# Kernel optimization log

Hardware: AMD Instinct MI355X
Metric: run time of the kernel (lower is better)

The kernel has to match this reference:

```python
import jax, jax.numpy as jnp
import numpy as np

M = 4096   # nodes per layer (also number of input nodes)
L = 32     # internal layers
K = 64     # in-degree of each internal node


def setup_inputs() -> dict:
    key = jax.random.key(0)
    k_x, k_wi, k_bi, k_w, k_b, k_g = jax.random.split(key, 6)
    x = jax.random.normal(k_x, (M, 1), dtype=jnp.float32)
    w_in = jax.random.normal(k_wi, (M, 1), dtype=jnp.float32)
    b_in = jax.random.normal(k_bi, (M,), dtype=jnp.float32)
    # scale internal weights so sigmoid(K-term dot) is not fully saturated
    w = jax.random.normal(k_w, (L, M, K), dtype=jnp.float32) * 0.05
    b = jax.random.normal(k_b, (L, M), dtype=jnp.float32)
    # predecessor indices into the previous layer's value vector
    igraf = jax.random.randint(k_g, (L, M, K), 0, M, dtype=jnp.int32)
    return {"x": x, "w_in": w_in, "b_in": b_in, "w": w, "b": b, "igraf": igraf}


def reference(x, w_in, b_in, w, b, igraf):
    # input nodes: relu(Linear(1,1)) applied to each scalar input, vectorized
    v = jax.nn.relu(w_in[:, 0] * x[:, 0] + b_in)          # [M]
    # internal nodes, layer by layer (topological order):
    # each node gathers K predecessor values and applies sigmoid(Linear(K,1))
    for l in range(L):
        g = v[igraf[l]]                                   # [M, K] irregular gather
        v = jax.nn.sigmoid(jnp.einsum('mk,mk->m', w[l], g) + b[l])
    # original returns values[n_nodes - 1] (shape [1])
    return v[-1:]
```

## Files before the change

### kernel.cpp

```cpp
#include <hip/hip_runtime.h>

#define M 4096
#define L 32
#define K 64
#define NBLK 256
#define BLOCK 256
#define NPW 4
#define NPB 16
#define MK (M * K)
#define FB 0xAAAAAAAAu

__global__ __launch_bounds__(BLOCK)
void net_kernel(const float* __restrict__ x,
                const float* __restrict__ w_in,
                const float* __restrict__ b_in,
                const float* __restrict__ w,
                const float* __restrict__ b,
                const int* __restrict__ igraf,
                float* __restrict__ out,
                unsigned long long* __restrict__ buf)
{
    __shared__ float sv[2][M];

    const int tid  = threadIdx.x;
    const int blk  = blockIdx.x;
    const int wave = tid >> 6;
    const int lane = tid & 63;
    const int base = blk * NPB + wave * NPW;
    const bool lastblk = (blk == NBLK - 1);

    float wv[NPW]; int iv[NPW]; float breg = 0.0f;
    {
        const size_t b0 = (size_t)base * K + (size_t)lane;
        #pragma unroll
        for (int j = 0; j < NPW; ++j) {
            wv[j] = w[b0 + (size_t)j * K];
            iv[j] = igraf[b0 + (size_t)j * K];
        }
        if (lane < NPW) breg = b[base + lane];
    }

    #pragma unroll
    for (int j = 0; j < 4; ++j) {
        const int idx = tid + j * BLOCK;
        const float4 x4 = ((const float4*)x)[idx];
        const float4 wi = ((const float4*)w_in)[idx];
        const float4 bi = ((const float4*)b_in)[idx];
        float4 r;
        r.x = fmaxf(fmaf(wi.x, x4.x, bi.x), 0.0f);
        r.y = fmaxf(fmaf(wi.y, x4.y, bi.y), 0.0f);
        r.z = fmaxf(fmaf(wi.z, x4.z, bi.z), 0.0f);
        r.w = fmaxf(fmaf(wi.w, x4.w, bi.w), 0.0f);
        ((float4*)sv[0])[idx] = r;
    }
    __syncthreads();

    int cur = 0;
    for (int l = 0; l < L; ++l) {
        float p[NPW];
        #pragma unroll
        for (int j = 0; j < NPW; ++j) p[j] = wv[j] * sv[cur][iv[j]];

        #pragma unroll
        for (int j = 0; j < NPW; ++j) {
            #pragma unroll
            for (int off = 32; off > 0; off >>= 1)
                p[j] += __shfl_xor(p[j], off, 64);
        }

        float pj = p[0];
        pj = (lane == 1) ? p[1] : pj;
        pj = (lane == 2) ? p[2] : pj;
        pj = (lane == 3) ? p[3] : pj;
        const float val = 1.0f / (1.0f + __expf(-(pj + breg)));

        if (l == L - 1) {
            if (wave == 3 && lane == 3) out[0] = val;
            break;
        }

        const unsigned tag = FB + (unsigned)(l + 1);
        unsigned long long* bufr = buf + (size_t)((l + 1) & 1) * M;

        if (lane < NPW) {
            const unsigned long long pk =
                ((unsigned long long)tag << 32) |
                (unsigned long long)__float_as_uint(val);
            __hip_atomic_store(&bufr[base + lane], pk,
                               __ATOMIC_RELAXED, __HIP_MEMORY_SCOPE_AGENT);
        }

        if ((l == L - 2) && !lastblk) return;

        unsigned long long vals[16];
        #pragma unroll
        for (int j = 0; j < 16; ++j)
            vals[j] = __hip_atomic_load(&bufr[tid + j * BLOCK],
                                        __ATOMIC_RELAXED,
                                        __HIP_MEMORY_SCOPE_AGENT);

        if ((l + 2 < L) || lastblk) {
            const size_t nb = (size_t)(l + 1) * MK + (size_t)base * K + (size_t)lane;
            #pragma unroll
            for (int j = 0; j < NPW; ++j) {
                wv[j] = w[nb + (size_t)j * K];
                iv[j] = igraf[nb + (size_t)j * K];
            }
            if (lane < NPW) breg = b[(l + 1) * M + base + lane];
        }

        for (;;) {
            bool ok = true;
            #pragma unroll
            for (int j = 0; j < 16; ++j) {
                if ((unsigned)(vals[j] >> 32) != tag) {
                    ok = false;
                    vals[j] = __hip_atomic_load(&bufr[tid + j * BLOCK],
                                                __ATOMIC_RELAXED,
                                                __HIP_MEMORY_SCOPE_AGENT);
                }
            }
            if (ok) break;
            __builtin_amdgcn_s_sleep(1);
        }

        const int nxt = cur ^ 1;
        #pragma unroll
        for (int j = 0; j < 16; ++j)
            sv[nxt][tid + j * BLOCK] = __uint_as_float((unsigned)vals[j]);

        __syncthreads();
        cur = nxt;
    }
}

extern "C" void kernel_launch(void* const* d_in, const int* in_sizes, int n_in,
                              void* d_out, int out_size, void* d_ws, size_t ws_size,
                              hipStream_t stream) {
    const float* x     = (const float*)d_in[0];
    const float* w_in  = (const float*)d_in[1];
    const float* b_in  = (const float*)d_in[2];
    const float* wt    = (const float*)d_in[3];
    const float* b     = (const float*)d_in[4];
    const int*   igraf = (const int*)d_in[5];
    float*       out   = (float*)d_out;

    unsigned long long* buf = (unsigned long long*)d_ws;

    hipLaunchKernelGGL(net_kernel, dim3(NBLK), dim3(BLOCK), 0, stream,
                       x, w_in, b_in, wt, b, igraf, out, buf);
    (void)in_sizes; (void)n_in; (void)out_size; (void)ws_size;
}
```

Before: 189.8 us.

## Use fewer, larger blocks and prefetch weights several layers ahead

```diff
diff --git a/kernel.cpp b/kernel.cpp
--- a/kernel.cpp
+++ b/kernel.cpp
@@ -3,10 +3,11 @@
 #define M 4096
 #define L 32
 #define K 64
-#define NBLK 256
-#define BLOCK 256
+#define NBLK 64
+#define BLOCK 1024
 #define NPW 4
-#define NPB 16
+#define NPB 64
+#define D 4
 #define MK (M * K)
 #define FB 0xAAAAAAAAu
 
@@ -27,110 +28,126 @@
     const int wave = tid >> 6;
     const int lane = tid & 63;
     const int base = blk * NPB + wave * NPW;
-    const bool lastblk = (blk == NBLK - 1);
+    const bool finblk = (blk == NBLK - 1);
 
-    float wv[NPW]; int iv[NPW]; float breg = 0.0f;
-    {
-        const size_t b0 = (size_t)base * K + (size_t)lane;
+    float4 x4[4], wi[4], bi[4];
+    #pragma unroll
+    for (int j = 0; j < 4; ++j) {
+        const int idx = tid + j * BLOCK;
+        x4[j] = ((const float4*)x)[idx];
+        wi[j] = ((const float4*)w_in)[idx];
+        bi[j] = ((const float4*)b_in)[idx];
+    }
+    __asm__ volatile("" ::: "memory");
+
+    float wbuf[D][NPW]; int ibuf[D][NPW]; float bbuf[D];
+    #pragma unroll
+    for (int d = 0; d < D; ++d) {
+        const size_t o = (size_t)d * MK + (size_t)base * K + (size_t)lane;
         #pragma unroll
         for (int j = 0; j < NPW; ++j) {
-            wv[j] = w[b0 + (size_t)j * K];
-            iv[j] = igraf[b0 + (size_t)j * K];
+            wbuf[d][j] = w[o + (size_t)j * K];
+            ibuf[d][j] = igraf[o + (size_t)j * K];
         }
-        if (lane < NPW) breg = b[base + lane];
+        bbuf[d] = (lane < NPW) ? b[d * M + base + lane] : 0.0f;
     }
 
     #pragma unroll
     for (int j = 0; j < 4; ++j) {
         const int idx = tid + j * BLOCK;
-        const float4 x4 = ((const float4*)x)[idx];
-        const float4 wi = ((const float4*)w_in)[idx];
-        const float4 bi = ((const float4*)b_in)[idx];
         float4 r;
-        r.x = fmaxf(fmaf(wi.x, x4.x, bi.x), 0.0f);
-        r.y = fmaxf(fmaf(wi.y, x4.y, bi.y), 0.0f);
-        r.z = fmaxf(fmaf(wi.z, x4.z, bi.z), 0.0f);
-        r.w = fmaxf(fmaf(wi.w, x4.w, bi.w), 0.0f);
+        r.x = fmaxf(fmaf(wi[j].x, x4[j].x, bi[j].x), 0.0f);
+        r.y = fmaxf(fmaf(wi[j].y, x4[j].y, bi[j].y), 0.0f);
+        r.z = fmaxf(fmaf(wi[j].z, x4[j].z, bi[j].z), 0.0f);
+        r.w = fmaxf(fmaf(wi[j].w, x4[j].w, bi[j].w), 0.0f);
         ((float4*)sv[0])[idx] = r;
     }
     __syncthreads();
 
     int cur = 0;
-    for (int l = 0; l < L; ++l) {
-        float p[NPW];
+    for (int g = 0; g < L / D; ++g) {
         #pragma unroll
-        for (int j = 0; j < NPW; ++j) p[j] = wv[j] * sv[cur][iv[j]];
+        for (int s = 0; s < D; ++s) {
+            const int l = g * D + s;
 
-        #pragma unroll
-        for (int j = 0; j < NPW; ++j) {
+            float p[NPW];
             #pragma unroll
-            for (int off = 32; off > 0; off >>= 1)
-                p[j] += __shfl_xor(p[j], off, 64);
-        }
+            for (int j = 0; j < NPW; ++j)
+                p[j] = wbuf[s][j] * sv[cur][ibuf[s][j]];
 
-        float pj = p[0];
-        pj = (lane == 1) ? p[1] : pj;
-        pj = (lane == 2) ? p[2] : pj;
-        pj = (lane == 3) ? p[3] : pj;
-        const float val = 1.0f / (1.0f + __expf(-(pj + breg)));
-
-        if (l == L - 1) {
-            if (wave == 3 && lane == 3) out[0] = val;
-            break;
-        }
-
-        const unsigned tag = FB + (unsigned)(l + 1);
-        unsigned long long* bufr = buf + (size_t)((l + 1) & 1) * M;
-
-        if (lane < NPW) {
-            const unsigned long long pk =
-                ((unsigned long long)tag << 32) |
-                (unsigned long long)__float_as_uint(val);
-            __hip_atomic_store(&bufr[base + lane], pk,
-                               __ATOMIC_RELAXED, __HIP_MEMORY_SCOPE_AGENT);
-        }
-
-        if ((l == L - 2) && !lastblk) return;
-
-        unsigned long long vals[16];
-        #pragma unroll
-        for (int j = 0; j < 16; ++j)
-            vals[j] = __hip_atomic_load(&bufr[tid + j * BLOCK],
-                                        __ATOMIC_RELAXED,
-                                        __HIP_MEMORY_SCOPE_AGENT);
-
-        if ((l + 2 < L) || lastblk) {
-            const size_t nb = (size_t)(l + 1) * MK + (size_t)base * K + (size_t)lane;
             #pragma unroll
             for (int j = 0; j < NPW; ++j) {
-                wv[j] = w[nb + (size_t)j * K];
-                iv[j] = igraf[nb + (size_t)j * K];
+                #pragma unroll
+                for (int off = 32; off > 0; off >>= 1)
+                    p[j] += __shfl_xor(p[j], off, 64);
             }
-            if (lane < NPW) breg = b[(l + 1) * M + base + lane];
+
+            float pj = p[0];
+            pj = (lane == 1) ? p[1] : pj;
+            pj = (lane == 2) ? p[2] : pj;
+            pj = (lane == 3) ? p[3] : pj;
+            const float val = 1.0f / (1.0f + __expf(-(pj + bbuf[s])));
+
+            if (l == L - 1) {
+                if (wave == 15 && lane == 3) out[0] = val;
+                return;
+            }
+
+            const unsigned tag = FB + (unsigned)(l + 1);
+            unsigned long long* bufr = buf + (size_t)((l + 1) & 1) * M;
+
+            if (lane < NPW) {
+                const unsigned long long pk =
+                    ((unsigned long long)tag << 32) |
+                    (unsigned long long)__float_as_uint(val);
+                __hip_atomic_store(&bufr[base + lane], pk,
+                                   __ATOMIC_RELAXED, __HIP_MEMORY_SCOPE_AGENT);
+            }
+
+            if (l == L - 2 && !finblk) return;
+
+            unsigned long long vals[4];
+            #pragma unroll
+            for (int j = 0; j < 4; ++j)
+                vals[j] = __hip_atomic_load(&bufr[tid + j * BLOCK],
+                                            __ATOMIC_RELAXED,
+                                            __HIP_MEMORY_SCOPE_AGENT);
+            __asm__ volatile("" ::: "memory");
+
+            if (l + D < L) {
+                const size_t o = (size_t)(l + D) * MK
+                               + (size_t)base * K + (size_t)lane;
+                #pragma unroll
+                for (int j = 0; j < NPW; ++j) {
+                    wbuf[s][j] = w[o + (size_t)j * K];
+                    ibuf[s][j] = igraf[o + (size_t)j * K];
+                }
+                if (lane < NPW) bbuf[s] = b[(l + D) * M + base + lane];
+            }
+
+            for (;;) {
+                bool ok = true;
+                #pragma unroll
+                for (int j = 0; j < 4; ++j) {
+                    if ((unsigned)(vals[j] >> 32) != tag) {
+                        ok = false;
+                        vals[j] = __hip_atomic_load(&bufr[tid + j * BLOCK],
+                                                    __ATOMIC_RELAXED,
+                                                    __HIP_MEMORY_SCOPE_AGENT);
+                    }
+                }
+                if (ok) break;
+                __builtin_amdgcn_s_sleep(1);
+            }
+
+            const int nxt = cur ^ 1;
+            #pragma unroll
+            for (int j = 0; j < 4; ++j)
+                sv[nxt][tid + j * BLOCK] =
+                    __uint_as_float((unsigned)vals[j]);
+            __syncthreads();
+            cur = nxt;
         }
-
-        for (;;) {
-            bool ok = true;
-            #pragma unroll
-            for (int j = 0; j < 16; ++j) {
-                if ((unsigned)(vals[j] >> 32) != tag) {
-                    ok = false;
-                    vals[j] = __hip_atomic_load(&bufr[tid + j * BLOCK],
-                                                __ATOMIC_RELAXED,
-                                                __HIP_MEMORY_SCOPE_AGENT);
-                }
-            }
-            if (ok) break;
-            __builtin_amdgcn_s_sleep(1);
-        }
-
-        const int nxt = cur ^ 1;
-        #pragma unroll
-        for (int j = 0; j < 16; ++j)
-            sv[nxt][tid + j * BLOCK] = __uint_as_float((unsigned)vals[j]);
-
-        __syncthreads();
-        cur = nxt;
     }
 }
 
```

Measured after the change: 221.4 us. 16.7% more time.

## Replace per-value tagged polling with per-block flags and layer-indexed buffers

Applied to the files above, without the earlier changes.

```diff
diff --git a/kernel.cpp b/kernel.cpp
--- a/kernel.cpp
+++ b/kernel.cpp
@@ -8,7 +8,6 @@
 #define NPW 4
 #define NPB 16
 #define MK (M * K)
-#define FB 0xAAAAAAAAu
 
 __global__ __launch_bounds__(BLOCK)
 void net_kernel(const float* __restrict__ x,
@@ -18,7 +17,8 @@
                 const float* __restrict__ b,
                 const int* __restrict__ igraf,
                 float* __restrict__ out,
-                unsigned long long* __restrict__ buf)
+                unsigned char* __restrict__ flags,
+                float* __restrict__ bufs)
 {
     __shared__ float sv[2][M];
 
@@ -76,28 +76,25 @@
 
         if (l == L - 1) {
             if (wave == 3 && lane == 3) out[0] = val;
-            break;
+            return;
         }
 
-        const unsigned tag = FB + (unsigned)(l + 1);
-        unsigned long long* bufr = buf + (size_t)((l + 1) & 1) * M;
+        const int r = l + 1;
+        float* bufr = bufs + (size_t)r * M;
 
         if (lane < NPW) {
-            const unsigned long long pk =
-                ((unsigned long long)tag << 32) |
-                (unsigned long long)__float_as_uint(val);
-            __hip_atomic_store(&bufr[base + lane], pk,
+            float old = __hip_atomic_exchange(&bufr[base + lane], val,
+                                              __ATOMIC_RELAXED,
+                                              __HIP_MEMORY_SCOPE_AGENT);
+            __asm__ volatile("" :: "v"(old));
+        }
+        __syncthreads();
+
+        if (tid == 0)
+            __hip_atomic_store(&flags[blk], (unsigned char)r,
                                __ATOMIC_RELAXED, __HIP_MEMORY_SCOPE_AGENT);
-        }
 
-        if ((l == L - 2) && !lastblk) return;
-
-        unsigned long long vals[16];
-        #pragma unroll
-        for (int j = 0; j < 16; ++j)
-            vals[j] = __hip_atomic_load(&bufr[tid + j * BLOCK],
-                                        __ATOMIC_RELAXED,
-                                        __HIP_MEMORY_SCOPE_AGENT);
+        if (l == L - 2 && !lastblk) return;
 
         if ((l + 2 < L) || lastblk) {
             const size_t nb = (size_t)(l + 1) * MK + (size_t)base * K + (size_t)lane;
@@ -109,26 +106,24 @@
             if (lane < NPW) breg = b[(l + 1) * M + base + lane];
         }
 
-        for (;;) {
-            bool ok = true;
-            #pragma unroll
-            for (int j = 0; j < 16; ++j) {
-                if ((unsigned)(vals[j] >> 32) != tag) {
-                    ok = false;
-                    vals[j] = __hip_atomic_load(&bufr[tid + j * BLOCK],
-                                                __ATOMIC_RELAXED,
-                                                __HIP_MEMORY_SCOPE_AGENT);
-                }
+        {
+            const unsigned tgt = 0x01010101u * (unsigned)r;
+            const unsigned* f4 = (const unsigned*)flags;
+            for (;;) {
+                const unsigned v = __hip_atomic_load(&f4[lane],
+                        __ATOMIC_RELAXED, __HIP_MEMORY_SCOPE_AGENT);
+                if (__ballot(v == tgt) == ~0ull) break;
+                __builtin_amdgcn_s_sleep(4);
             }
-            if (ok) break;
-            __builtin_amdgcn_s_sleep(1);
+            __asm__ volatile("" ::: "memory");
         }
 
         const int nxt = cur ^ 1;
         #pragma unroll
-        for (int j = 0; j < 16; ++j)
-            sv[nxt][tid + j * BLOCK] = __uint_as_float((unsigned)vals[j]);
-
+        for (int j = 0; j < 4; ++j) {
+            const int idx = tid + j * BLOCK;
+            ((float4*)sv[nxt])[idx] = ((const float4*)bufr)[idx];
+        }
         __syncthreads();
         cur = nxt;
     }
@@ -145,9 +140,10 @@
     const int*   igraf = (const int*)d_in[5];
     float*       out   = (float*)d_out;
 
-    unsigned long long* buf = (unsigned long long*)d_ws;
+    unsigned char* flags = (unsigned char*)d_ws;
+    float*         bufs  = (float*)((char*)d_ws + 4096);
 
     hipLaunchKernelGGL(net_kernel, dim3(NBLK), dim3(BLOCK), 0, stream,
-                       x, w_in, b_in, wt, b, igraf, out, buf);
+                       x, w_in, b_in, wt, b, igraf, out, flags, bufs);
     (void)in_sizes; (void)n_in; (void)out_size; (void)ws_size;
 }
```

After: 301.6 us. +58.9%, slower.
